# Kernel tuning notes

Hardware: AMD Instinct MI355X
Metric: run time of the kernel (lower is better)

Reference implementation:

```python
import jax, jax.numpy as jnp
import numpy as np

NUM_GRAPHS = 32      # equal-sized graphs; batch = node_id // (N // NUM_GRAPHS)
RATIO = 0.5
NEG_SLOPE = 0.2
BN_EPS = 1e-5


def setup_inputs() -> dict:
    key = jax.random.key(0)
    k0, k1, k2, k3, k4 = jax.random.split(key, 5)
    N, Cin, Cout, E = 65536, 256, 128, 1048576
    x = jax.random.normal(k0, (N, Cin), dtype=jnp.float32)
    # edges with no self loops (remove_self_loops is then a no-op)
    src = jax.random.randint(k1, (E,), 0, N, dtype=jnp.int32)
    off = jax.random.randint(k2, (E,), 1, N, dtype=jnp.int32)
    dst = (src + off) % N
    edge_index = jnp.stack([src, dst])  # [2, E], row0=source j, row1=target i
    batch = jnp.repeat(jnp.arange(NUM_GRAPHS, dtype=jnp.int32), N // NUM_GRAPHS)
    # glorot init for weight and att
    s_w = float(np.sqrt(6.0 / (Cin + Cout)))
    W = jax.random.uniform(k3, (Cin, Cout), jnp.float32, -s_w, s_w)
    s_a = float(np.sqrt(6.0 / (1 + 2 * Cout)))
    att = jax.random.uniform(k4, (2 * Cout,), jnp.float32, -s_a, s_a)
    bn_gamma = jnp.ones((Cout,), jnp.float32)
    bn_beta = jnp.zeros((Cout,), jnp.float32)
    return {"x": x, "W": W, "att": att, "bn_gamma": bn_gamma, "bn_beta": bn_beta,
            "edge_index": edge_index, "batch": batch, "bn": 1}


def reference(x, W, att, bn_gamma, bn_beta, edge_index, batch, bn):
    N = x.shape[0]
    C = W.shape[1]
    loops = jnp.arange(N, dtype=edge_index.dtype)
    src = jnp.concatenate([edge_index[0], loops])  # source j
    dst = jnp.concatenate([edge_index[1], loops])  # target i
    xw = x @ W  # [N, C]
    # alpha_e = (cat[x_i, x_j] * att).sum(-1) = x_i.att[:C] + x_j.att[C:]
    a_i = xw @ att[:C]
    a_j = xw @ att[C:]
    alpha = a_i[dst] + a_j[src]
    alpha = jnp.where(alpha >= 0, alpha, NEG_SLOPE * alpha)  # leaky_relu
    # edge softmax grouped by target node (edge_index_i)
    seg_max = jax.ops.segment_max(alpha, dst, num_segments=N)
    seg_max = jnp.where(jnp.isfinite(seg_max), seg_max, 0.0)
    ex = jnp.exp(alpha - seg_max[dst])
    denom = jax.ops.segment_sum(ex, dst, num_segments=N)  # >0 (self loops)
    alpha = ex / denom[dst]
    # per-source-node attention mass
    alpha_sum = jax.ops.segment_sum(alpha, src, num_segments=N)
    # per-graph top-k node selection (equal graph sizes -> static shapes)
    n = N // NUM_GRAPHS
    k = int(n * RATIO)
    scores = alpha_sum.reshape(NUM_GRAPHS, n)
    _, idx = jax.lax.top_k(scores, k)                       # [B, k]
    perm = (idx + jnp.arange(NUM_GRAPHS)[:, None] * n).reshape(-1)  # global node ids
    topk_batch = jnp.repeat(jnp.arange(NUM_GRAPHS, dtype=batch.dtype), k)
    # delete_node: keep only edges whose endpoints both survive
    keep = jnp.zeros((N,), bool).at[perm].set(True)
    emask = keep[src] & keep[dst]
    scale = jnp.where(emask, alpha, 0.0)
    msg = xw[src] * scale[:, None]                          # [E+N, C] gather
    out = jax.ops.segment_sum(msg, dst, num_segments=N)     # scatter-add aggr
    out_final = out[perm]                                   # [B*k, C]
    if bn:
        mu = out_final.mean(axis=0)
        var = out_final.var(axis=0)
        out_final = (out_final - mu) * jax.lax.rsqrt(var + BN_EPS) * bn_gamma + bn_beta
    return (out_final, perm, topk_batch)
```

## Files before the change

### kernel.cpp

```cpp
#include <hip/hip_runtime.h>
#include <math.h>

#define CIN 256
#define COUT 128
#define NGRAPH 32
#define NCHUNK 256

__global__ __launch_bounds__(256) void gemm_csr(const float* __restrict__ x,
                                                const float* __restrict__ W,
                                                float* __restrict__ xw,
                                                const int* __restrict__ esrc,
                                                const int* __restrict__ edst,
                                                int* __restrict__ deg,
                                                unsigned short* __restrict__ csr_j,
                                                int E, int M, int nGemm) {
    __shared__ float xs[32][68];
    __shared__ float ws[32][132];
    if ((int)blockIdx.x < nGemm) {
        int t = threadIdx.x;
        int bm0 = blockIdx.x * 64;
        int tx = t & 15;
        int ty = t >> 4;
        float acc[4][8];
#pragma unroll
        for (int i = 0; i < 4; ++i)
#pragma unroll
            for (int j = 0; j < 8; ++j) acc[i][j] = 0.0f;

        for (int kc = 0; kc < CIN / 32; ++kc) {
            int k0 = kc * 32;
            {
                int ml = t >> 2, kq = (t & 3) * 8;
                const float* sp = x + (size_t)(bm0 + ml) * CIN + k0 + kq;
                float4 v0 = ((const float4*)sp)[0];
                float4 v1 = ((const float4*)sp)[1];
                xs[kq + 0][ml] = v0.x;  xs[kq + 1][ml] = v0.y;
                xs[kq + 2][ml] = v0.z;  xs[kq + 3][ml] = v0.w;
                xs[kq + 4][ml] = v1.x;  xs[kq + 5][ml] = v1.y;
                xs[kq + 6][ml] = v1.z;  xs[kq + 7][ml] = v1.w;
            }
            {
                int kl = t >> 3, n0 = (t & 7) * 16;
                const float* sp = W + (size_t)(k0 + kl) * COUT + n0;
#pragma unroll
                for (int w4 = 0; w4 < 4; ++w4)
                    *(float4*)&ws[kl][n0 + 4 * w4] = *(const float4*)(sp + 4 * w4);
            }
            __syncthreads();
#pragma unroll 4
            for (int kk = 0; kk < 32; ++kk) {
                float aa[4], bb[8];
                *(float4*)&aa[0] = *(float4*)&xs[kk][tx * 4];
                *(float4*)&bb[0] = *(float4*)&ws[kk][ty * 8];
                *(float4*)&bb[4] = *(float4*)&ws[kk][ty * 8 + 4];
#pragma unroll
                for (int i = 0; i < 4; ++i)
#pragma unroll
                    for (int j = 0; j < 8; ++j) acc[i][j] += aa[i] * bb[j];
            }
            __syncthreads();
        }
#pragma unroll
        for (int i = 0; i < 4; ++i) {
            float* dp = xw + (size_t)(bm0 + tx * 4 + i) * COUT + ty * 8;
            float4 s0 = {acc[i][0], acc[i][1], acc[i][2], acc[i][3]};
            float4 s1 = {acc[i][4], acc[i][5], acc[i][6], acc[i][7]};
            *(float4*)dp = s0;
            *(float4*)(dp + 4) = s1;
        }
        return;
    }
    int bid = blockIdx.x - nGemm;
    int k = bid & 7;
    int r = bid >> 3;
    int lo = k << 13, hi = lo + 8192;
    int pairs = M >> 1;
    int chunkP = (pairs + NCHUNK - 1) / NCHUNK;
    int p0 = r * chunkP;
    int p1 = p0 + chunkP; if (p1 > pairs) p1 = pairs;
    for (int p = p0 + threadIdx.x; p < p1; p += 256) {
        int e0 = p * 2;
        int i0, j0, i1, j1;
        if (e0 < E) {
            int2 js = *(const int2*)(esrc + e0);
            int2 is = *(const int2*)(edst + e0);
            j0 = js.x; j1 = js.y; i0 = is.x; i1 = is.y;
        } else {
            i0 = j0 = e0 - E; i1 = j1 = e0 + 1 - E;
        }
        if (i0 >= lo && i0 < hi) {
            int s0 = atomicAdd(&deg[i0], 1);
            if (s0 < 64) csr_j[(i0 << 6) + s0] = (unsigned short)j0;
        }
        if (i1 >= lo && i1 < hi) {
            int s1 = atomicAdd(&deg[i1], 1);
            if (s1 < 64) csr_j[(i1 << 6) + s1] = (unsigned short)j1;
        }
    }
}

__global__ __launch_bounds__(256) void aij32_kernel(const float* __restrict__ xw,
                                                    const float* __restrict__ att,
                                                    float* __restrict__ a_i,
                                                    float* __restrict__ a_j) {
    __shared__ float sa[2 * COUT];
    int t = threadIdx.x;
    sa[t] = att[t];
    __syncthreads();
    int n = blockIdx.x * 256 + t;
    const float* row = xw + (size_t)n * COUT;
    float ai = 0.0f, aj = 0.0f;
#pragma unroll 8
    for (int c = 0; c < COUT; c += 4) {
        float4 f = *(const float4*)(row + c);
        ai += f.x * sa[c];     aj += f.x * sa[COUT + c];
        ai += f.y * sa[c + 1]; aj += f.y * sa[COUT + c + 1];
        ai += f.z * sa[c + 2]; aj += f.z * sa[COUT + c + 2];
        ai += f.w * sa[c + 3]; aj += f.w * sa[COUT + c + 3];
    }
    a_i[n] = ai;
    a_j[n] = aj;
}

__global__ __launch_bounds__(256) void node_softmax(const int* __restrict__ deg,
                                                    const unsigned short* __restrict__ csr_j,
                                                    const float* __restrict__ a_i,
                                                    const float* __restrict__ a_j,
                                                    float* __restrict__ mbuf,
                                                    float* __restrict__ dbuf,
                                                    double* __restrict__ asum) {
    int t = threadIdx.x;
    int g = t & 15;
    int node = blockIdx.x * 16 + (t >> 4);
    int d = deg[node];
    if (d > 64) d = 64;
    float ai = a_i[node];
    int base = node << 6;
    ushort4 jraw = *(const ushort4*)(csr_j + base + 4 * g);
    unsigned short js[4] = {jraw.x, jraw.y, jraw.z, jraw.w};
    float l[4];
    int jj[4];
    float lm = -INFINITY;
#pragma unroll
    for (int q = 0; q < 4; ++q) {
        int p = 4 * g + q;
        if (p < d) {
            int j = (int)js[q];
            float lv = ai + a_j[j];
            lv = (lv >= 0.0f) ? lv : 0.2f * lv;
            jj[q] = j; l[q] = lv;
            lm = fmaxf(lm, lv);
        } else {
            jj[q] = -1;
        }
    }
#pragma unroll
    for (int mk = 1; mk < 16; mk <<= 1)
        lm = fmaxf(lm, __shfl_xor(lm, mk, 16));
    float ex[4];
    double ds = 0.0;
#pragma unroll
    for (int q = 0; q < 4; ++q) {
        if (jj[q] >= 0) {
            ex[q] = expf(l[q] - lm);
            ds += (double)ex[q];
        }
    }
#pragma unroll
    for (int mk = 1; mk < 16; mk <<= 1)
        ds += __shfl_xor(ds, mk, 16);
    float df = (float)ds;
#pragma unroll
    for (int q = 0; q < 4; ++q) {
        if (jj[q] >= 0) {
            float al = ex[q] / df;
            atomicAdd(&asum[jj[q]], (double)al);
        }
    }
    if (g == 0) { mbuf[node] = lm; dbuf[node] = df; }
}

__global__ __launch_bounds__(256) void rank_kernel(const double* __restrict__ asum,
                                                   int* __restrict__ rank,
                                                   float* __restrict__ out,
                                                   int* __restrict__ perm_int,
                                                   double* __restrict__ bnacc,
                                                   int perG, int kSel,
                                                   int permOff, int tbOff) {
    __shared__ float sc[2048];
    int bpg = perG >> 8;
    int g = blockIdx.x / bpg;
    int sub = blockIdx.x - g * bpg;
    int t = threadIdx.x;
    if (blockIdx.x == 0) bnacc[t] = 0.0;
    for (int q = t; q < perG; q += 256)
        sc[q] = (float)asum[g * perG + q];
    __syncthreads();
    int m = sub * 256 + t;
    float s = sc[m];
    int r = 0;
#pragma unroll 4
    for (int q4 = 0; q4 < 2048; q4 += 4) {
        float4 f = *(const float4*)&sc[q4];
        r += (int)((f.x > s) || (f.x == s && (q4 + 0) < m));
        r += (int)((f.y > s) || (f.y == s && (q4 + 1) < m));
        r += (int)((f.z > s) || (f.z == s && (q4 + 2) < m));
        r += (int)((f.w > s) || (f.w == s && (q4 + 3) < m));
    }
    int node = g * perG + m;
    if (r < kSel) {
        int pos = g * kSel + r;
        rank[node] = pos;
        perm_int[pos] = node;
        out[permOff + pos] = (float)node;
        out[tbOff + pos] = (float)g;
    } else {
        rank[node] = -1;
    }
}

__global__ __launch_bounds__(256) void aggr_kernel(const int* __restrict__ perm_int,
                                                   const int* __restrict__ deg,
                                                   const unsigned short* __restrict__ csr_j,
                                                   const int* __restrict__ rank,
                                                   const float* __restrict__ a_i,
                                                   const float* __restrict__ a_j,
                                                   const float* __restrict__ mbuf,
                                                   const float* __restrict__ dbuf,
                                                   const float* __restrict__ xw,
                                                   float* __restrict__ outf, int R) {
    int wid = (int)((blockIdx.x * 256u + threadIdx.x) >> 6);
    int lane = threadIdx.x & 63;
    if (wid >= R) return;
    int node = perm_int[wid];
    int d = deg[node];
    if (d > 64) d = 64;
    float ai = a_i[node];
    float m = mbuf[node];
    float df = dbuf[node];
    int base = node << 6;
    int jv = 0, kv = 0;
    float alv = 0.0f;
    if (lane < d) {
        jv = (int)csr_j[base + lane];
        if (rank[jv] >= 0) {
            float l = ai + a_j[jv];
            l = (l >= 0.0f) ? l : 0.2f * l;
            alv = expf(l - m) / df;
            kv = 1;
        }
    }
    float2 acc = {0.0f, 0.0f};
    for (int p = 0; p < d; ++p) {
        int keep = __shfl(kv, p, 64);
        if (!keep) continue;
        int j = __shfl(jv, p, 64);
        float al = __shfl(alv, p, 64);
        float2 xv = *(const float2*)(xw + (size_t)j * COUT + lane * 2);
        acc.x += xv.x * al;
        acc.y += xv.y * al;
    }
    *(float2*)(outf + (size_t)wid * COUT + lane * 2) = acc;
}

__global__ __launch_bounds__(256) void bn_stats(const float* __restrict__ outf,
                                                double* __restrict__ acc, int R) {
    int t = threadIdx.x;
    int c = t & 127;
    int r0 = blockIdx.x * 2 + (t >> 7);
    double s = 0.0, s2 = 0.0;
    for (int r = r0; r < R; r += 512) {
        double v = (double)outf[(size_t)r * COUT + c];
        s += v; s2 += v * v;
    }
    atomicAdd(&acc[c], s);
    atomicAdd(&acc[128 + c], s2);
}

__global__ void bn_apply(float* __restrict__ outf, const double* __restrict__ acc,
                         const float* __restrict__ gamma, const float* __restrict__ beta,
                         const int* __restrict__ bnflag, int R) {
    int idx = blockIdx.x * blockDim.x + threadIdx.x;
    if (idx >= R * COUT) return;
    if (*bnflag == 0) return;
    int c = idx & 127;
    double invR = 1.0 / (double)R;
    double mu = acc[c] * invR;
    double var = acc[128 + c] * invR - mu * mu;
    double inv = 1.0 / sqrt(var + 1e-5);
    outf[idx] = (float)(((double)outf[idx] - mu) * inv * (double)gamma[c] + (double)beta[c]);
}

extern "C" void kernel_launch(void* const* d_in, const int* in_sizes, int n_in,
                              void* d_out, int out_size, void* d_ws, size_t ws_size,
                              hipStream_t stream) {
    const float* x     = (const float*)d_in[0];
    const float* W     = (const float*)d_in[1];
    const float* att   = (const float*)d_in[2];
    const float* gamma = (const float*)d_in[3];
    const float* beta  = (const float*)d_in[4];
    const int*   eidx  = (const int*)d_in[5];
    const int*   bnfl  = (const int*)d_in[7];

    const int N = in_sizes[0] / CIN;
    const int E = in_sizes[5] / 2;
    const int M = E + N;
    const int perG = N / NGRAPH;
    const int kSel = perG / 2;
    const int R = NGRAPH * kSel;
    const int permOff = R * COUT;
    const int tbOff = permOff + R;

    const int* esrc = eidx;
    const int* edst = eidx + E;

    char* w = (char*)d_ws;
    float*  xw     = (float*)w;             w += (size_t)N * COUT * 4;
    float*  a_i    = (float*)w;             w += (size_t)N * 4;
    float*  a_j    = (float*)w;             w += (size_t)N * 4;
    int*    deg    = (int*)w;               w += (size_t)N * 4;
    double* asum   = (double*)w;            w += (size_t)N * 8;
    float*  mbuf   = (float*)w;             w += (size_t)N * 4;
    float*  dbuf   = (float*)w;             w += (size_t)N * 4;
    unsigned short* csr_j = (unsigned short*)w; w += (size_t)N * 64 * 2;
    int*    rank   = (int*)w;               w += (size_t)N * 4;
    int*    perm_int = (int*)w;             w += (size_t)R * 4;
    double* bnacc  = (double*)w;            w += 256 * 8;

    float* out = (float*)d_out;

    hipMemsetAsync(deg, 0, (size_t)N * (4 + 8), stream);

    const int nGemm = N / 64;
    gemm_csr<<<nGemm + NCHUNK * 8, 256, 0, stream>>>(x, W, xw, esrc, edst,
                                                     deg, csr_j, E, M, nGemm);

    aij32_kernel<<<N / 256, 256, 0, stream>>>(xw, att, a_i, a_j);

    node_softmax<<<N / 16, 256, 0, stream>>>(deg, csr_j, a_i, a_j, mbuf, dbuf, asum);

    rank_kernel<<<NGRAPH * (perG >> 8), 256, 0, stream>>>(asum, rank, out, perm_int,
                                                          bnacc, perG, kSel, permOff, tbOff);

    aggr_kernel<<<(R * 64 + 255) / 256, 256, 0, stream>>>(perm_int, deg, csr_j, rank,
                                                          a_i, a_j, mbuf, dbuf, xw, out, R);

    bn_stats<<<256, 256, 0, stream>>>(out, bnacc, R);
    bn_apply<<<(R * COUT + 255) / 256, 256, 0, stream>>>(out, bnacc, gamma, beta, bnfl, R);
}
```

Baseline: 372.8 us.

## Replace fp64 atomic alpha_sum scatter with source-indexed CSR gather kernel

Builds a second per-source CSR (outdeg/csr_i) during the edge-bucketing pass and computes alpha_sum with a new gather kernel that recomputes each edge's softmax weight from a_i, a_j, max and denominator, instead of scattering double-precision atomics from node_softmax. This removes roughly a million fp64 atomic adds and the memset of asum. The cost is double the CSR-build atomics and stores, an extra kernel launch, and extra random gathers of a_i, mbuf and dbuf.

```diff
diff --git a/kernel.cpp b/kernel.cpp
--- a/kernel.cpp
+++ b/kernel.cpp
@@ -13,6 +13,8 @@
                                                 const int* __restrict__ edst,
                                                 int* __restrict__ deg,
                                                 unsigned short* __restrict__ csr_j,
+                                                int* __restrict__ outdeg,
+                                                unsigned short* __restrict__ csr_i,
                                                 int E, int M, int nGemm) {
     __shared__ float xs[32][68];
     __shared__ float ws[32][132];
@@ -96,6 +98,14 @@
             int s1 = atomicAdd(&deg[i1], 1);
             if (s1 < 64) csr_j[(i1 << 6) + s1] = (unsigned short)j1;
         }
+        if (j0 >= lo && j0 < hi) {
+            int s0 = atomicAdd(&outdeg[j0], 1);
+            if (s0 < 64) csr_i[(j0 << 6) + s0] = (unsigned short)i0;
+        }
+        if (j1 >= lo && j1 < hi) {
+            int s1 = atomicAdd(&outdeg[j1], 1);
+            if (s1 < 64) csr_i[(j1 << 6) + s1] = (unsigned short)i1;
+        }
     }
 }
 
@@ -127,8 +137,7 @@
                                                     const float* __restrict__ a_i,
                                                     const float* __restrict__ a_j,
                                                     float* __restrict__ mbuf,
-                                                    float* __restrict__ dbuf,
-                                                    double* __restrict__ asum) {
+                                                    float* __restrict__ dbuf) {
     int t = threadIdx.x;
     int g = t & 15;
     int node = blockIdx.x * 16 + (t >> 4);
@@ -157,27 +166,53 @@
 #pragma unroll
     for (int mk = 1; mk < 16; mk <<= 1)
         lm = fmaxf(lm, __shfl_xor(lm, mk, 16));
-    float ex[4];
     double ds = 0.0;
 #pragma unroll
     for (int q = 0; q < 4; ++q) {
         if (jj[q] >= 0) {
-            ex[q] = expf(l[q] - lm);
-            ds += (double)ex[q];
+            float ex = expf(l[q] - lm);
+            ds += (double)ex;
         }
     }
 #pragma unroll
     for (int mk = 1; mk < 16; mk <<= 1)
         ds += __shfl_xor(ds, mk, 16);
     float df = (float)ds;
+    if (g == 0) { mbuf[node] = lm; dbuf[node] = df; }
+}
+
+__global__ __launch_bounds__(256) void node_asum(const int* __restrict__ outdeg,
+                                                 const unsigned short* __restrict__ csr_i,
+                                                 const float* __restrict__ a_i,
+                                                 const float* __restrict__ a_j,
+                                                 const float* __restrict__ mbuf,
+                                                 const float* __restrict__ dbuf,
+                                                 double* __restrict__ asum) {
+    int t = threadIdx.x;
+    int g = t & 15;
+    int node = blockIdx.x * 16 + (t >> 4);
+    int d = outdeg[node];
+    if (d > 64) d = 64;
+    float aj = a_j[node];
+    int base = node << 6;
+    ushort4 iraw = *(const ushort4*)(csr_i + base + 4 * g);
+    unsigned short is[4] = {iraw.x, iraw.y, iraw.z, iraw.w};
+    double ds = 0.0;
 #pragma unroll
     for (int q = 0; q < 4; ++q) {
-        if (jj[q] >= 0) {
-            float al = ex[q] / df;
-            atomicAdd(&asum[jj[q]], (double)al);
-        }
-    }
-    if (g == 0) { mbuf[node] = lm; dbuf[node] = df; }
+        int p = 4 * g + q;
+        if (p < d) {
+            int ii = (int)is[q];
+            float l = a_i[ii] + aj;
+            l = (l >= 0.0f) ? l : 0.2f * l;
+            float al = expf(l - mbuf[ii]) / dbuf[ii];
+            ds += (double)al;
+        }
+    }
+#pragma unroll
+    for (int mk = 1; mk < 16; mk <<= 1)
+        ds += __shfl_xor(ds, mk, 16);
+    if (g == 0) asum[node] = ds;
 }
 
 __global__ __launch_bounds__(256) void rank_kernel(const double* __restrict__ asum,
@@ -319,25 +354,30 @@
     float*  a_i    = (float*)w;             w += (size_t)N * 4;
     float*  a_j    = (float*)w;             w += (size_t)N * 4;
     int*    deg    = (int*)w;               w += (size_t)N * 4;
+    int*    outdeg = (int*)w;               w += (size_t)N * 4;
     double* asum   = (double*)w;            w += (size_t)N * 8;
     float*  mbuf   = (float*)w;             w += (size_t)N * 4;
     float*  dbuf   = (float*)w;             w += (size_t)N * 4;
     unsigned short* csr_j = (unsigned short*)w; w += (size_t)N * 64 * 2;
+    unsigned short* csr_i = (unsigned short*)w; w += (size_t)N * 64 * 2;
     int*    rank   = (int*)w;               w += (size_t)N * 4;
     int*    perm_int = (int*)w;             w += (size_t)R * 4;
     double* bnacc  = (double*)w;            w += 256 * 8;
 
     float* out = (float*)d_out;
 
-    hipMemsetAsync(deg, 0, (size_t)N * (4 + 8), stream);
+    hipMemsetAsync(deg, 0, (size_t)N * (4 + 4), stream);
 
     const int nGemm = N / 64;
     gemm_csr<<<nGemm + NCHUNK * 8, 256, 0, stream>>>(x, W, xw, esrc, edst,
-                                                     deg, csr_j, E, M, nGemm);
+                                                     deg, csr_j, outdeg, csr_i,
+                                                     E, M, nGemm);
 
     aij32_kernel<<<N / 256, 256, 0, stream>>>(xw, att, a_i, a_j);
 
-    node_softmax<<<N / 16, 256, 0, stream>>>(deg, csr_j, a_i, a_j, mbuf, dbuf, asum);
+    node_softmax<<<N / 16, 256, 0, stream>>>(deg, csr_j, a_i, a_j, mbuf, dbuf);
+
+    node_asum<<<N / 16, 256, 0, stream>>>(outdeg, csr_i, a_i, a_j, mbuf, dbuf, asum);
 
     rank_kernel<<<NGRAPH * (perG >> 8), 256, 0, stream>>>(asum, rank, out, perm_int,
                                                           bnacc, perG, kSel, permOff, tbOff);
```

New measurement: 388.5 us. +4.2%, slower.
